# Performance work log

Hardware: AMD Instinct MI355X
Metric: run time of the kernel (lower is better)

Reference implementation:

```python
import jax, jax.numpy as jnp
import numpy as np

B, T, N, L = 128, 2048, 64, 256
NEG = -1e30  # safe -inf surrogate (avoids inf-inf NaNs in gradients)


def setup_inputs() -> dict:
    key = jax.random.key(0)
    k1, k2, k3, k4 = jax.random.split(key, 4)
    inputs = jax.random.normal(k1, (B, T, N), dtype=jnp.float32)
    target = jax.random.randint(k2, (B, L), 0, N, dtype=jnp.int32)
    # valid target lengths in [1, L]
    target_size = jax.random.randint(k3, (B,), 1, L + 1, dtype=jnp.int32)
    # module initializes trans to zeros; use small random values for a nontrivial reference
    trans = jax.random.normal(k4, (N, N), dtype=jnp.float32) * 0.1
    return {"input": inputs, "target": target, "target_size": target_size, "trans": trans}


def _fcc(inputs, trans):
    # Full-connection (partition) score: logsumexp over ALL label paths.
    # alpha_t[b, j] = input[b, t, j] + logsumexp_i( alpha_{t-1}[b, i] + trans[j, i] )
    def step(alpha, x_t):  # alpha: [B, N], x_t: [B, N]
        alpha = x_t + jax.nn.logsumexp(alpha[:, None, :] + trans[None, :, :], axis=2)
        return alpha, None

    alpha0 = inputs[:, 0, :]
    xs = jnp.swapaxes(inputs, 0, 1)[1:]  # [T-1, B, N]
    alphaT, _ = jax.lax.scan(step, alpha0, xs)
    return jax.nn.logsumexp(alphaT, axis=1)  # [B]


def _fac(inputs, trans, target, target_size):
    # Forced-alignment score: logsumexp over alignments emitting target labels
    # in order, each repeated >= 1 time (ASG: no blank).
    b = inputs.shape[0]
    b_idx = jnp.arange(b)
    trans_self = trans[target, target]                 # [B, L] stay on label l
    trans_move = trans[target[:, 1:], target[:, :-1]]  # [B, L-1] advance l-1 -> l
    neg_col = jnp.full((b, 1), NEG, dtype=inputs.dtype)

    alpha0 = jnp.full(target.shape, NEG, dtype=inputs.dtype)
    alpha0 = alpha0.at[:, 0].set(inputs[b_idx, 0, target[:, 0]])

    def step(alpha, x_t):  # alpha: [B, L], x_t: [B, N]
        emit = jnp.take_along_axis(x_t, target, axis=1)  # [B, L]
        stay = alpha + trans_self
        move = jnp.concatenate([neg_col, alpha[:, :-1] + trans_move], axis=1)
        alpha = emit + jnp.logaddexp(stay, move)
        return alpha, None

    xs = jnp.swapaxes(inputs, 0, 1)[1:]  # [T-1, B, N]
    alphaT, _ = jax.lax.scan(step, alpha0, xs)
    return alphaT[b_idx, target_size - 1]  # [B]


def reference(input, target, target_size, trans):
    # ASG loss = FullConnection (partition) - ForceAlignment (target score), per batch element.
    return _fcc(input, trans) - _fac(input, trans, target, target_size)
```

## Files before the change

### kernel.cpp

```cpp
#include <hip/hip_runtime.h>

#define B_ 128
#define T_ 2048
#define N_ 64
#define L_ 256
#define NEGV (-1e30f)
#define PITCH 72
#define LOG2E 1.4426950408889634f
#define LN2   0.6931471805599453f

typedef short  s16x4 __attribute__((ext_vector_type(4)));
typedef short  s16x8 __attribute__((ext_vector_type(8)));
typedef float  f32x4 __attribute__((ext_vector_type(4)));
typedef float  f32x16 __attribute__((ext_vector_type(16)));
typedef unsigned int u32x2 __attribute__((ext_vector_type(2)));
typedef unsigned int u32x4 __attribute__((ext_vector_type(4)));

__device__ __forceinline__ short f2bf_rne(float f) {
    unsigned u = __float_as_uint(f);
    unsigned r = (u + 0x7FFFu + ((u >> 16) & 1u)) >> 16;
    return (short)r;
}
__device__ __forceinline__ float bf2f(unsigned short u) {
    return __uint_as_float(((unsigned)u) << 16);
}
__device__ __forceinline__ float bperm(int byteaddr, float v) {
    return __int_as_float(__builtin_amdgcn_ds_bpermute(byteaddr, __float_as_int(v)));
}
__device__ __forceinline__ float lse2b(float p, float q) {
    float mx = fmaxf(p, q);
    float t  = __builtin_amdgcn_exp2f(-fabsf(p - q));
    return mx + __builtin_amdgcn_logf(1.f + t);
}
__device__ __forceinline__ unsigned cvtpk_bf16(float lo, float hi) {
    unsigned r;
    asm("v_cvt_pk_bf16_f32 %0, %1, %2" : "=v"(r) : "v"(lo), "v"(hi));
    return r;
}
__device__ __forceinline__ void plswap32(unsigned &x, unsigned &y) {
    asm("v_permlane32_swap_b32 %0, %1" : "+v"(x), "+v"(y));
}

__global__ __launch_bounds__(256, 2) void asg_k1(
    const float* __restrict__ x,
    const int*   __restrict__ target,
    const int*   __restrict__ tsize,
    const float* __restrict__ trans,
    float* __restrict__ ws_c,
    unsigned short* __restrict__ ws_R,
    float* __restrict__ ws_v,
    float* __restrict__ ws_w)
{
    __shared__ float evbuf[4][N_];
    const int wid  = threadIdx.x >> 6;
    const int lane = threadIdx.x & 63;
    const int W    = blockIdx.x * 4 + wid;

    if (W < 128) {
        const int b  = W;
        const float* __restrict__ xb = x + (size_t)b * T_ * N_;
        const int l0 = lane * 4;
        int tga[4]; float slf[4], mv[4], a[4];
        #pragma unroll
        for (int j = 0; j < 4; ++j) {
            const int tv = target[b * L_ + l0 + j];
            tga[j] = tv << 2;
            slf[j] = trans[tv * N_ + tv] * LOG2E;
            if (j > 0) mv[j] = trans[tv * N_ + (target[b * L_ + l0 + j - 1])] * LOG2E;
            a[j] = NEGV;
        }
        const int tR  = target[b * L_ + ((l0 - 1 >= 0) ? l0 - 1 : 0)];
        const int tR1 = target[b * L_ + ((l0 - 2 >= 0) ? l0 - 2 : 0)];
        const int tgR = tR << 2;
        const float slfR = trans[tR * N_ + tR] * LOG2E;
        const float mvR  = trans[tR * N_ + tR1] * LOG2E;
        mv[0] = trans[(tga[0] >> 2) * N_ + tR] * LOG2E;
        if (lane == 0) a[0] = xb[tga[0] >> 2] * LOG2E;
        float red = NEGV;
        const int upA = ((lane == 0) ? 0 : lane - 1) << 2;

        float xr[16];
        #pragma unroll
        for (int i = 0; i < 16; ++i) xr[i] = xb[(size_t)(1 + i) * N_ + lane];
        float sc = xr[0] * LOG2E;
        float eR = bperm(tgR, sc);
        float e0 = bperm(tga[0], sc), e1 = bperm(tga[1], sc),
              e2 = bperm(tga[2], sc), e3 = bperm(tga[3], sc);
        float bp = bperm(upA, a[2]);

        #define FWD_STEP(i, rp, RF)                                             \
        {                                                                       \
            const float ceR = eR, c0 = e0, c1 = e1, c2 = e2, c3 = e3;           \
            float scn = xr[((i) + 1) & 15] * LOG2E;                             \
            eR = bperm(tgR, scn);                                               \
            e0 = bperm(tga[0], scn); e1 = bperm(tga[1], scn);                   \
            e2 = bperm(tga[2], scn); e3 = bperm(tga[3], scn);                   \
            if (RF) xr[i] = (rp)[lane];                                         \
            const float n0 = lse2b(a[0] + slf[0], red  + mv[0]) + c0;           \
            const float n1 = lse2b(a[1] + slf[1], a[0] + mv[1]) + c1;           \
            const float n2 = lse2b(a[2] + slf[2], a[1] + mv[2]) + c2;           \
            const float n3 = lse2b(a[3] + slf[3], a[2] + mv[3]) + c3;           \
            const float nr = lse2b(red + slfR,    bp   + mvR)   + ceR;          \
            bp = bperm(upA, n2);                                                \
            a[0] = n0; a[1] = n1; a[2] = n2; a[3] = n3;                         \
            red = (lane == 0) ? NEGV : nr;                                      \
        }
        for (int u = 0; u < 63; ++u) {
            const float* __restrict__ xp = xb + (size_t)(16 * u + 17) * N_;
            #pragma unroll
            for (int i = 0; i < 16; ++i) FWD_STEP(i, xp + i * N_, true);
        }
        #pragma unroll
        for (int i = 0; i < 15; ++i) FWD_STEP(i, xb, false);
        #undef FWD_STEP
        *(float4*)(ws_v + b * 256 + l0) = make_float4(a[0], a[1], a[2], a[3]);
    } else if (W < 256) {
        const int b  = W - 128;
        const float* __restrict__ xb = x + (size_t)b * T_ * N_;
        const int l0 = lane * 4;
        const int lt = tsize[b] - 1;
        int tga[4]; float slf[4], mvin[4], a[4];
        #pragma unroll
        for (int j = 0; j < 4; ++j) {
            const int tv = target[b * L_ + l0 + j];
            tga[j] = tv << 2;
            slf[j] = trans[tv * N_ + tv] * LOG2E;
            if (j > 0) mvin[j] = trans[tv * N_ + (target[b * L_ + l0 + j - 1])] * LOG2E;
            a[j] = (l0 + j == lt) ? 0.f : NEGV;
        }
        const int tR  = target[b * L_ + ((l0 + 4 <= L_ - 1) ? l0 + 4 : L_ - 1)];
        const int tR2 = target[b * L_ + ((l0 + 5 <= L_ - 1) ? l0 + 5 : L_ - 1)];
        const int tgR = tR << 2, tgR2 = tR2 << 2;
        const float slfR = trans[tR * N_ + tR] * LOG2E;
        const float mvR  = trans[tR * N_ + (tga[3] >> 2)] * LOG2E;
        const float mvR2 = trans[tR2 * N_ + tR] * LOG2E;
        float red = (l0 + 4 == lt) ? 0.f : NEGV;
        const int dnA = ((lane == 63) ? 63 : lane + 1) << 2;

        float xr[16];
        #pragma unroll
        for (int i = 0; i < 16; ++i) xr[i] = xb[(size_t)(2047 - i) * N_ + lane];
        float sc = xr[0] * LOG2E;
        float eR = bperm(tgR, sc), eR2 = bperm(tgR2, sc);
        float e0 = bperm(tga[0], sc), e1 = bperm(tga[1], sc),
              e2 = bperm(tga[2], sc), e3 = bperm(tga[3], sc);
        float bp = bperm(dnA, a[1]);

        #define BWD_STEP(i, rp, RF)                                             \
        {                                                                       \
            const float ceR = eR, ceR2 = eR2, c0 = e0, c1 = e1, c2 = e2, c3 = e3;\
            float scn = xr[((i) + 1) & 15] * LOG2E;                             \
            eR = bperm(tgR, scn); eR2 = bperm(tgR2, scn);                       \
            e0 = bperm(tga[0], scn); e1 = bperm(tga[1], scn);                   \
            e2 = bperm(tga[2], scn); e3 = bperm(tga[3], scn);                   \
            if (RF) xr[i] = (rp)[lane];                                         \
            const float t0 = a[0] + c0, t1 = a[1] + c1, t2 = a[2] + c2,         \
                        t3 = a[3] + c3, tr = red + ceR;                         \
            const float n0 = lse2b(t0 + slf[0], t1 + mvin[1]);                  \
            const float n1 = lse2b(t1 + slf[1], t2 + mvin[2]);                  \
            const float n2 = lse2b(t2 + slf[2], t3 + mvin[3]);                  \
            const float n3 = lse2b(t3 + slf[3], tr + mvR);                      \
            const float nr = lse2b(tr + slfR, bp + ceR2 + mvR2);                \
            bp = bperm(dnA, n1);                                                \
            a[0] = n0; a[1] = n1; a[2] = n2; a[3] = n3;                         \
            red = (lane == 63) ? NEGV : nr;                                     \
        }
        for (int u = 0; u < 63; ++u) {
            const float* __restrict__ xp = xb + (size_t)(2047 - 16 * u - 16) * N_;
            #pragma unroll
            for (int i = 0; i < 16; ++i) BWD_STEP(i, xp - (size_t)i * N_, true);
        }
        #pragma unroll
        for (int i = 0; i < 16; ++i) BWD_STEP(i, xb, false);
        #undef BWD_STEP
        *(float4*)(ws_w + b * 256 + l0) = make_float4(a[0], a[1], a[2], a[3]);
    } else {
        const int task = W - 256;
        const int b = task >> 5, k = task & 31;
        const int lane31 = lane & 31, hi = lane >> 5;
        const float* __restrict__ xb = x + (size_t)b * T_ * N_;
        const int t0 = k * 64;
        float* __restrict__ evb = evbuf[wid];

        s16x8 Ahat[2][4];
        float rsum[2];
        #pragma unroll
        for (int r = 0; r < 2; ++r) {
            float rs = 0.f;
            const float* tp = trans + (32 * r + lane31) * N_;
            #pragma unroll
            for (int kt = 0; kt < 4; ++kt) {
                const float* tq = tp + 16 * kt + 8 * hi;
                float4 ta = *(const float4*)tq;
                float4 tb = *(const float4*)(tq + 4);
                float v0 = __expf(ta.x), v1 = __expf(ta.y),
                      v2 = __expf(ta.z), v3 = __expf(ta.w);
                float v4 = __expf(tb.x), v5 = __expf(tb.y),
                      v6 = __expf(tb.z), v7 = __expf(tb.w);
                s16x8 af;
                af[0] = f2bf_rne(v0); af[1] = f2bf_rne(v1);
                af[2] = f2bf_rne(v2); af[3] = f2bf_rne(v3);
                af[4] = f2bf_rne(v4); af[5] = f2bf_rne(v5);
                af[6] = f2bf_rne(v6); af[7] = f2bf_rne(v7);
                rs += ((v0 + v1) + (v2 + v3)) + ((v4 + v5) + (v6 + v7));
                Ahat[r][kt] = af;
            }
            rsum[r] = rs;
        }
        rsum[0] += __shfl_xor(rsum[0], 32);
        rsum[1] += __shfl_xor(rsum[1], 32);
        float rmax = fmaxf(rsum[0], rsum[1]);
        #pragma unroll
        for (int o = 16; o > 0; o >>= 1) rmax = fmaxf(rmax, __shfl_xor(rmax, o));
        const float LS = __logf(rmax);

        s16x8 Pf[4][2];
        #pragma unroll
        for (int kt = 0; kt < 4; ++kt)
            #pragma unroll
            for (int c = 0; c < 2; ++c) {
                s16x8 pf;
                #pragma unroll
                for (int j = 0; j < 8; ++j)
                    pf[j] = (16 * kt + 8 * hi + j == 32 * c + lane31)
                              ? (short)0x3F80 : (short)0;
                Pf[kt][c] = pf;
            }

        const f32x16 z16 = {};
        f32x16 Y00 = {}, Y01 = {}, Y10 = {}, Y11 = {};
        float xpre[4];
        #pragma unroll
        for (int d = 0; d < 4; ++d)
            xpre[d] = xb[(size_t)(t0 + 1 + d) * N_ + lane];
        float c_acc = 0.f;

        #define MM(af, bf, cf) __builtin_amdgcn_mfma_f32_32x32x16_bf16(af, bf, cf, 0, 0, 0)
        #define REDIST(kt, c, Yv)                                               \
        {                                                                       \
            unsigned P0 = cvtpk_bf16(Yv[8*((kt)&1) + 0], Yv[8*((kt)&1) + 1]);   \
            unsigned P1 = cvtpk_bf16(Yv[8*((kt)&1) + 2], Yv[8*((kt)&1) + 3]);   \
            unsigned Q0 = cvtpk_bf16(Yv[8*((kt)&1) + 4], Yv[8*((kt)&1) + 5]);   \
            unsigned Q1 = cvtpk_bf16(Yv[8*((kt)&1) + 6], Yv[8*((kt)&1) + 7]);   \
            plswap32(P0, Q0); plswap32(P1, Q1);                                 \
            u32x4 uv; uv[0] = P0; uv[1] = P1; uv[2] = Q0; uv[3] = Q1;           \
            Pf[kt][c] = __builtin_bit_cast(s16x8, uv);                          \
        }

        #pragma unroll 1
        for (int u = 0; u < 16; ++u) {
            #pragma unroll
            for (int i = 0; i < 4; ++i) {
                const int s = 4 * u + i;
                const int t = t0 + 1 + s;
                if (t < T_) {
                    const float xt = xpre[i];
                    int tp2 = t + 4; if (tp2 > T_ - 1) tp2 = T_ - 1;
                    xpre[i] = xb[(size_t)tp2 * N_ + lane];
                    const float gt = __uint_as_float(
                        __builtin_amdgcn_readfirstlane(__float_as_uint(xt))) + LS;
                    c_acc += gt;
                    evb[lane] = __expf(xt - gt);
                    float4 E[2][4];
                    #pragma unroll
                    for (int r = 0; r < 2; ++r)
                        #pragma unroll
                        for (int q = 0; q < 4; ++q)
                            E[r][q] = *(const float4*)&evb[32 * r + 8 * q + 4 * hi];
                    Y00 = MM(Ahat[0][0], Pf[0][0], z16);
                    Y01 = MM(Ahat[0][0], Pf[0][1], z16);
                    Y10 = MM(Ahat[1][0], Pf[0][0], z16);
                    Y11 = MM(Ahat[1][0], Pf[0][1], z16);
                    #pragma unroll
                    for (int kt = 1; kt < 4; ++kt) {
                        Y00 = MM(Ahat[0][kt], Pf[kt][0], Y00);
                        Y01 = MM(Ahat[0][kt], Pf[kt][1], Y01);
                        Y10 = MM(Ahat[1][kt], Pf[kt][0], Y10);
                        Y11 = MM(Ahat[1][kt], Pf[kt][1], Y11);
                    }
                    #pragma unroll
                    for (int q = 0; q < 4; ++q) {
                        Y00[4*q+0] *= E[0][q].x; Y00[4*q+1] *= E[0][q].y;
                        Y00[4*q+2] *= E[0][q].z; Y00[4*q+3] *= E[0][q].w;
                        Y01[4*q+0] *= E[0][q].x; Y01[4*q+1] *= E[0][q].y;
                        Y01[4*q+2] *= E[0][q].z; Y01[4*q+3] *= E[0][q].w;
                        Y10[4*q+0] *= E[1][q].x; Y10[4*q+1] *= E[1][q].y;
                        Y10[4*q+2] *= E[1][q].z; Y10[4*q+3] *= E[1][q].w;
                        Y11[4*q+0] *= E[1][q].x; Y11[4*q+1] *= E[1][q].y;
                        Y11[4*q+2] *= E[1][q].z; Y11[4*q+3] *= E[1][q].w;
                    }
                    REDIST(0, 0, Y00); REDIST(0, 1, Y01);
                    REDIST(1, 0, Y00); REDIST(1, 1, Y01);
                    REDIST(2, 0, Y10); REDIST(2, 1, Y11);
                    REDIST(3, 0, Y10); REDIST(3, 1, Y11);
                }
            }
        }
        #undef REDIST
        #undef MM

        unsigned short* dst = ws_R + (size_t)(b * 32 + k) * 4096;
        #pragma unroll
        for (int q = 0; q < 4; ++q)
            #pragma unroll
            for (int m = 0; m < 4; ++m) {
                const int reg = 4 * q + m;
                const int rw  = 8 * q + 4 * hi + m;
                dst[(rw     ) * 64 + lane31     ] = (unsigned short)f2bf_rne(Y00[reg]);
                dst[(rw     ) * 64 + 32 + lane31] = (unsigned short)f2bf_rne(Y01[reg]);
                dst[(32 + rw) * 64 + lane31     ] = (unsigned short)f2bf_rne(Y10[reg]);
                dst[(32 + rw) * 64 + 32 + lane31] = (unsigned short)f2bf_rne(Y11[reg]);
            }
        if (lane == 0) ws_c[b * 32 + k] = c_acc;
    }
}

__global__ __launch_bounds__(128) void asg_k2(
    const float* __restrict__ x,
    const float* __restrict__ ws_c,
    const unsigned short* __restrict__ ws_R,
    const float* __restrict__ ws_v,
    const float* __restrict__ ws_w,
    float* __restrict__ out)
{
    __shared__ short rb[2][N_ * PITCH];
    __shared__ __align__(16) float sa[N_];
    __shared__ float sres[2];
    const int b = blockIdx.x, tid = threadIdx.x, lane = tid & 63;

    if (tid < 64) {
        float a0 = x[(size_t)b * T_ * N_ + lane];
        float m0 = a0;
        #pragma unroll
        for (int o = 32; o > 0; o >>= 1) m0 = fmaxf(m0, __shfl_xor(m0, o));
        float  a  = __expf(a0 - m0);
        double Cd = (double)m0;

        const unsigned short* Rb = ws_R + (size_t)b * 32 * 4096;
        const int frow = (lane >> 3), fcol = (lane & 7) * 8;
        {
            #pragma unroll
            for (int q = 0; q < 8; ++q) {
                s16x8 v = *(const s16x8*)(Rb + lane * 8 + 512 * q);
                *(s16x8*)&rb[0][(frow + 8 * q) * PITCH + fcol] = v;
            }
        }
        for (int kk = 0; kk < 32; ++kk) {
            const int kn = (kk < 31) ? kk + 1 : 31;
            s16x8 nv[8];
            #pragma unroll
            for (int q = 0; q < 8; ++q)
                nv[q] = *(const s16x8*)(Rb + (size_t)kn * 4096 + lane * 8 + 512 * q);

            sa[lane] = a;
            float4 sav[16];
            #pragma unroll
            for (int q = 0; q < 16; ++q) sav[q] = ((const float4*)sa)[q];

            float acc4[4] = {0.f, 0.f, 0.f, 0.f};
            #pragma unroll
            for (int u = 0; u < 8; ++u) {
                s16x8 rr = *(const s16x8*)&rb[kk & 1][lane * PITCH + u * 8];
                const float4 s0 = sav[2 * u], s1 = sav[2 * u + 1];
                acc4[0] = fmaf(bf2f((unsigned short)rr[0]), s0.x, acc4[0]);
                acc4[1] = fmaf(bf2f((unsigned short)rr[1]), s0.y, acc4[1]);
                acc4[2] = fmaf(bf2f((unsigned short)rr[2]), s0.z, acc4[2]);
                acc4[3] = fmaf(bf2f((unsigned short)rr[3]), s0.w, acc4[3]);
                acc4[0] = fmaf(bf2f((unsigned short)rr[4]), s1.x, acc4[0]);
                acc4[1] = fmaf(bf2f((unsigned short)rr[5]), s1.y, acc4[1]);
                acc4[2] = fmaf(bf2f((unsigned short)rr[6]), s1.z, acc4[2]);
                acc4[3] = fmaf(bf2f((unsigned short)rr[7]), s1.w, acc4[3]);
            }
            float acc = (acc4[0] + acc4[1]) + (acc4[2] + acc4[3]);
            float rm = acc;
            #pragma unroll
            for (int o = 32; o > 0; o >>= 1) rm = fmaxf(rm, __shfl_xor(rm, o));
            a = acc / rm;
            Cd += (double)(__logf(rm) + ws_c[b * 32 + kk]);

            #pragma unroll
            for (int q = 0; q < 8; ++q)
                *(s16x8*)&rb[(kk + 1) & 1][(frow + 8 * q) * PITCH + fcol] = nv[q];
        }
        float ssum = a;
        #pragma unroll
        for (int o = 32; o > 0; o >>= 1) ssum += __shfl_xor(ssum, o);
        if (lane == 0) sres[0] = (float)(Cd + (double)__logf(ssum));
    } else {
        float4 v4 = ((const float4*)(ws_v + b * 256))[lane];
        float4 w4 = ((const float4*)(ws_w + b * 256))[lane];
        const float s0 = v4.x + w4.x, s1 = v4.y + w4.y,
                    s2 = v4.z + w4.z, s3 = v4.w + w4.w;
        float m = fmaxf(fmaxf(s0, s1), fmaxf(s2, s3));
        #pragma unroll
        for (int o = 32; o > 0; o >>= 1) m = fmaxf(m, __shfl_xor(m, o));
        float sum = __builtin_amdgcn_exp2f(s0 - m) + __builtin_amdgcn_exp2f(s1 - m)
                  + __builtin_amdgcn_exp2f(s2 - m) + __builtin_amdgcn_exp2f(s3 - m);
        #pragma unroll
        for (int o = 32; o > 0; o >>= 1) sum += __shfl_xor(sum, o);
        if (lane == 0) sres[1] = (m + __builtin_amdgcn_logf(sum)) * LN2;
    }
    __syncthreads();
    if (tid == 0) out[b] = sres[0] - sres[1];
}

extern "C" void kernel_launch(void* const* d_in, const int* in_sizes, int n_in,
                              void* d_out, int out_size, void* d_ws, size_t ws_size,
                              hipStream_t stream) {
    (void)in_sizes; (void)n_in; (void)out_size; (void)ws_size;
    const float* xin    = (const float*)d_in[0];
    const int*   target = (const int*)  d_in[1];
    const int*   tsz    = (const int*)  d_in[2];
    const float* trans  = (const float*)d_in[3];
    float* out = (float*)d_out;

    float*          ws_c = (float*)d_ws;
    unsigned short* ws_R = (unsigned short*)((char*)d_ws + 16384);
    float*          ws_v = (float*)((char*)d_ws + 16384 + 33554432);
    float*          ws_w = (float*)((char*)d_ws + 16384 + 33554432 + 131072);

    asg_k1<<<dim3(1088), dim3(256), 0, stream>>>(xin, target, tsz, trans,
                                                 ws_c, ws_R, ws_v, ws_w);
    asg_k2<<<dim3(B_), dim3(128), 0, stream>>>(xin, ws_c, ws_R, ws_v, ws_w, out);
}
```

Before: 286.3 us.

## Spread FAC waves one per block, gather emissions directly, deepen K2 prefetch

The forced-alignment forward and backward waves now get one block each (wave 0 of blocks 0-255), and the FCC chunk tasks are remapped onto the remaining waves. Inside the alignment recurrence, the per-lane coalesced row load plus five or six ds_bpermute shuffles per step is replaced by direct gathered global loads of the needed emission values, prefetched four steps ahead in a register ring. The LOG2E scaling is folded into an fma. In the K2 combine loop, bf16 R tiles are now prefetched two iterations ahead with two register buffers, to hide global-load latency. The gather loads are uncoalesced and raise register use, and isolating the latency-bound waves changes occupancy and block balance.

```diff
diff --git a/kernel.cpp b/kernel.cpp
--- a/kernel.cpp
+++ b/kernel.cpp
@@ -54,128 +54,130 @@
     __shared__ float evbuf[4][N_];
     const int wid  = threadIdx.x >> 6;
     const int lane = threadIdx.x & 63;
-    const int W    = blockIdx.x * 4 + wid;
-
-    if (W < 128) {
-        const int b  = W;
+    const int bx   = blockIdx.x;
+    const bool isfac = (bx < 256) && (wid == 0);
+
+    if (isfac && bx < 128) {
+        const int b  = bx;
         const float* __restrict__ xb = x + (size_t)b * T_ * N_;
         const int l0 = lane * 4;
-        int tga[4]; float slf[4], mv[4], a[4];
+        int tg[4]; float slf[4], mv[4], a[4];
         #pragma unroll
         for (int j = 0; j < 4; ++j) {
             const int tv = target[b * L_ + l0 + j];
-            tga[j] = tv << 2;
+            tg[j] = tv;
             slf[j] = trans[tv * N_ + tv] * LOG2E;
             if (j > 0) mv[j] = trans[tv * N_ + (target[b * L_ + l0 + j - 1])] * LOG2E;
             a[j] = NEGV;
         }
         const int tR  = target[b * L_ + ((l0 - 1 >= 0) ? l0 - 1 : 0)];
         const int tR1 = target[b * L_ + ((l0 - 2 >= 0) ? l0 - 2 : 0)];
-        const int tgR = tR << 2;
         const float slfR = trans[tR * N_ + tR] * LOG2E;
         const float mvR  = trans[tR * N_ + tR1] * LOG2E;
-        mv[0] = trans[(tga[0] >> 2) * N_ + tR] * LOG2E;
-        if (lane == 0) a[0] = xb[tga[0] >> 2] * LOG2E;
+        mv[0] = trans[tg[0] * N_ + tR] * LOG2E;
+        if (lane == 0) a[0] = xb[tg[0]] * LOG2E;
         float red = NEGV;
+        float bp  = NEGV;
         const int upA = ((lane == 0) ? 0 : lane - 1) << 2;
 
-        float xr[16];
-        #pragma unroll
-        for (int i = 0; i < 16; ++i) xr[i] = xb[(size_t)(1 + i) * N_ + lane];
-        float sc = xr[0] * LOG2E;
-        float eR = bperm(tgR, sc);
-        float e0 = bperm(tga[0], sc), e1 = bperm(tga[1], sc),
-              e2 = bperm(tga[2], sc), e3 = bperm(tga[3], sc);
-        float bp = bperm(upA, a[2]);
-
-        #define FWD_STEP(i, rp, RF)                                             \
+        float E[4][5];
+        #pragma unroll
+        for (int d = 0; d < 4; ++d) {
+            const float* __restrict__ xp = xb + (size_t)(1 + d) * N_;
+            E[d][0] = xp[tg[0]]; E[d][1] = xp[tg[1]];
+            E[d][2] = xp[tg[2]]; E[d][3] = xp[tg[3]];
+            E[d][4] = xp[tR];
+        }
+
+        #define FWD_STEP(t, i)                                                  \
         {                                                                       \
-            const float ceR = eR, c0 = e0, c1 = e1, c2 = e2, c3 = e3;           \
-            float scn = xr[((i) + 1) & 15] * LOG2E;                             \
-            eR = bperm(tgR, scn);                                               \
-            e0 = bperm(tga[0], scn); e1 = bperm(tga[1], scn);                   \
-            e2 = bperm(tga[2], scn); e3 = bperm(tga[3], scn);                   \
-            if (RF) xr[i] = (rp)[lane];                                         \
-            const float n0 = lse2b(a[0] + slf[0], red  + mv[0]) + c0;           \
-            const float n1 = lse2b(a[1] + slf[1], a[0] + mv[1]) + c1;           \
-            const float n2 = lse2b(a[2] + slf[2], a[1] + mv[2]) + c2;           \
-            const float n3 = lse2b(a[3] + slf[3], a[2] + mv[3]) + c3;           \
-            const float nr = lse2b(red + slfR,    bp   + mvR)   + ceR;          \
+            const float c0 = E[i][0], c1 = E[i][1], c2 = E[i][2],               \
+                        c3 = E[i][3], cR = E[i][4];                             \
+            const int rw = ((t) + 4 <= 1023) ? (t) + 4 : 1023;                  \
+            const float* __restrict__ xp = xb + (size_t)rw * N_;                \
+            E[i][0] = xp[tg[0]]; E[i][1] = xp[tg[1]];                           \
+            E[i][2] = xp[tg[2]]; E[i][3] = xp[tg[3]];                           \
+            E[i][4] = xp[tR];                                                   \
+            const float n0 = fmaf(c0, LOG2E, lse2b(a[0] + slf[0], red  + mv[0]));\
+            const float n1 = fmaf(c1, LOG2E, lse2b(a[1] + slf[1], a[0] + mv[1]));\
+            const float n2 = fmaf(c2, LOG2E, lse2b(a[2] + slf[2], a[1] + mv[2]));\
+            const float n3 = fmaf(c3, LOG2E, lse2b(a[3] + slf[3], a[2] + mv[3]));\
+            const float nr = fmaf(cR, LOG2E, lse2b(red + slfR,    bp   + mvR)); \
             bp = bperm(upA, n2);                                                \
             a[0] = n0; a[1] = n1; a[2] = n2; a[3] = n3;                         \
             red = (lane == 0) ? NEGV : nr;                                      \
         }
-        for (int u = 0; u < 63; ++u) {
-            const float* __restrict__ xp = xb + (size_t)(16 * u + 17) * N_;
-            #pragma unroll
-            for (int i = 0; i < 16; ++i) FWD_STEP(i, xp + i * N_, true);
-        }
-        #pragma unroll
-        for (int i = 0; i < 15; ++i) FWD_STEP(i, xb, false);
+        for (int u = 0; u < 255; ++u) {
+            const int tb = 1 + 4 * u;
+            #pragma unroll
+            for (int i = 0; i < 4; ++i) FWD_STEP(tb + i, i);
+        }
+        FWD_STEP(1021, 0); FWD_STEP(1022, 1); FWD_STEP(1023, 2);
         #undef FWD_STEP
         *(float4*)(ws_v + b * 256 + l0) = make_float4(a[0], a[1], a[2], a[3]);
-    } else if (W < 256) {
-        const int b  = W - 128;
+    } else if (isfac) {
+        const int b  = bx - 128;
         const float* __restrict__ xb = x + (size_t)b * T_ * N_;
         const int l0 = lane * 4;
         const int lt = tsize[b] - 1;
-        int tga[4]; float slf[4], mvin[4], a[4];
+        int tg[4]; float slf[4], mvin[4], a[4];
         #pragma unroll
         for (int j = 0; j < 4; ++j) {
             const int tv = target[b * L_ + l0 + j];
-            tga[j] = tv << 2;
+            tg[j] = tv;
             slf[j] = trans[tv * N_ + tv] * LOG2E;
             if (j > 0) mvin[j] = trans[tv * N_ + (target[b * L_ + l0 + j - 1])] * LOG2E;
             a[j] = (l0 + j == lt) ? 0.f : NEGV;
         }
         const int tR  = target[b * L_ + ((l0 + 4 <= L_ - 1) ? l0 + 4 : L_ - 1)];
         const int tR2 = target[b * L_ + ((l0 + 5 <= L_ - 1) ? l0 + 5 : L_ - 1)];
-        const int tgR = tR << 2, tgR2 = tR2 << 2;
         const float slfR = trans[tR * N_ + tR] * LOG2E;
-        const float mvR  = trans[tR * N_ + (tga[3] >> 2)] * LOG2E;
+        const float mvR  = trans[tR * N_ + tg[3]] * LOG2E;
         const float mvR2 = trans[tR2 * N_ + tR] * LOG2E;
         float red = (l0 + 4 == lt) ? 0.f : NEGV;
+        float bp  = (l0 + 5 == lt) ? 0.f : NEGV;
         const int dnA = ((lane == 63) ? 63 : lane + 1) << 2;
 
-        float xr[16];
-        #pragma unroll
-        for (int i = 0; i < 16; ++i) xr[i] = xb[(size_t)(2047 - i) * N_ + lane];
-        float sc = xr[0] * LOG2E;
-        float eR = bperm(tgR, sc), eR2 = bperm(tgR2, sc);
-        float e0 = bperm(tga[0], sc), e1 = bperm(tga[1], sc),
-              e2 = bperm(tga[2], sc), e3 = bperm(tga[3], sc);
-        float bp = bperm(dnA, a[1]);
-
-        #define BWD_STEP(i, rp, RF)                                             \
+        float E[4][6];
+        #pragma unroll
+        for (int d = 0; d < 4; ++d) {
+            const float* __restrict__ xp = xb + (size_t)(2047 - d) * N_;
+            E[d][0] = xp[tg[0]]; E[d][1] = xp[tg[1]];
+            E[d][2] = xp[tg[2]]; E[d][3] = xp[tg[3]];
+            E[d][4] = xp[tR];    E[d][5] = xp[tR2];
+        }
+
+        #define BWD_STEP(t, i)                                                  \
         {                                                                       \
-            const float ceR = eR, ceR2 = eR2, c0 = e0, c1 = e1, c2 = e2, c3 = e3;\
-            float scn = xr[((i) + 1) & 15] * LOG2E;                             \
-            eR = bperm(tgR, scn); eR2 = bperm(tgR2, scn);                       \
-            e0 = bperm(tga[0], scn); e1 = bperm(tga[1], scn);                   \
-            e2 = bperm(tga[2], scn); e3 = bperm(tga[3], scn);                   \
-            if (RF) xr[i] = (rp)[lane];                                         \
-            const float t0 = a[0] + c0, t1 = a[1] + c1, t2 = a[2] + c2,         \
-                        t3 = a[3] + c3, tr = red + ceR;                         \
+            const float c0 = E[i][0], c1 = E[i][1], c2 = E[i][2],               \
+                        c3 = E[i][3], cR = E[i][4], cR2 = E[i][5];              \
+            const int rw = ((t) - 4 >= 1024) ? (t) - 4 : 1024;                  \
+            const float* __restrict__ xp = xb + (size_t)rw * N_;                \
+            E[i][0] = xp[tg[0]]; E[i][1] = xp[tg[1]];                           \
+            E[i][2] = xp[tg[2]]; E[i][3] = xp[tg[3]];                           \
+            E[i][4] = xp[tR];    E[i][5] = xp[tR2];                             \
+            const float t0 = fmaf(c0, LOG2E, a[0]), t1 = fmaf(c1, LOG2E, a[1]); \
+            const float t2 = fmaf(c2, LOG2E, a[2]), t3 = fmaf(c3, LOG2E, a[3]); \
+            const float tr = fmaf(cR, LOG2E, red);                              \
             const float n0 = lse2b(t0 + slf[0], t1 + mvin[1]);                  \
             const float n1 = lse2b(t1 + slf[1], t2 + mvin[2]);                  \
             const float n2 = lse2b(t2 + slf[2], t3 + mvin[3]);                  \
             const float n3 = lse2b(t3 + slf[3], tr + mvR);                      \
-            const float nr = lse2b(tr + slfR, bp + ceR2 + mvR2);                \
+            const float nr = lse2b(tr + slfR, bp + fmaf(cR2, LOG2E, mvR2));     \
             bp = bperm(dnA, n1);                                                \
             a[0] = n0; a[1] = n1; a[2] = n2; a[3] = n3;                         \
             red = (lane == 63) ? NEGV : nr;                                     \
         }
-        for (int u = 0; u < 63; ++u) {
-            const float* __restrict__ xp = xb + (size_t)(2047 - 16 * u - 16) * N_;
-            #pragma unroll
-            for (int i = 0; i < 16; ++i) BWD_STEP(i, xp - (size_t)i * N_, true);
-        }
-        #pragma unroll
-        for (int i = 0; i < 16; ++i) BWD_STEP(i, xb, false);
+        for (int u = 0; u < 256; ++u) {
+            const int tb = 2047 - 4 * u;
+            #pragma unroll
+            for (int i = 0; i < 4; ++i) BWD_STEP(tb - i, i);
+        }
         #undef BWD_STEP
         *(float4*)(ws_w + b * 256 + l0) = make_float4(a[0], a[1], a[2], a[3]);
     } else {
-        const int task = W - 256;
+        const int task = (bx < 256) ? (bx * 3 + wid - 1)
+                                    : (768 + (bx - 256) * 4 + wid);
         const int b = task >> 5, k = task & 31;
         const int lane31 = lane & 31, hi = lane >> 5;
         const float* __restrict__ xb = x + (size_t)b * T_ * N_;
@@ -345,22 +347,20 @@
                 *(s16x8*)&rb[0][(frow + 8 * q) * PITCH + fcol] = v;
             }
         }
-        for (int kk = 0; kk < 32; ++kk) {
-            const int kn = (kk < 31) ? kk + 1 : 31;
-            s16x8 nv[8];
-            #pragma unroll
-            for (int q = 0; q < 8; ++q)
-                nv[q] = *(const s16x8*)(Rb + (size_t)kn * 4096 + lane * 8 + 512 * q);
-
+        s16x8 nvA[8], nvB[8];
+        #pragma unroll
+        for (int q = 0; q < 8; ++q)
+            nvA[q] = *(const s16x8*)(Rb + (size_t)4096 + lane * 8 + 512 * q);
+
+        auto k2_step = [&](int kk, int bufi) {
             sa[lane] = a;
             float4 sav[16];
             #pragma unroll
             for (int q = 0; q < 16; ++q) sav[q] = ((const float4*)sa)[q];
-
             float acc4[4] = {0.f, 0.f, 0.f, 0.f};
             #pragma unroll
             for (int u = 0; u < 8; ++u) {
-                s16x8 rr = *(const s16x8*)&rb[kk & 1][lane * PITCH + u * 8];
+                s16x8 rr = *(const s16x8*)&rb[bufi][lane * PITCH + u * 8];
                 const float4 s0 = sav[2 * u], s1 = sav[2 * u + 1];
                 acc4[0] = fmaf(bf2f((unsigned short)rr[0]), s0.x, acc4[0]);
                 acc4[1] = fmaf(bf2f((unsigned short)rr[1]), s0.y, acc4[1]);
@@ -377,10 +377,25 @@
             for (int o = 32; o > 0; o >>= 1) rm = fmaxf(rm, __shfl_xor(rm, o));
             a = acc / rm;
             Cd += (double)(__logf(rm) + ws_c[b * 32 + kk]);
-
+        };
+
+        for (int kk = 0; kk < 32; kk += 2) {
+            const int kA = (kk + 2 < 32) ? kk + 2 : 31;
             #pragma unroll
             for (int q = 0; q < 8; ++q)
-                *(s16x8*)&rb[(kk + 1) & 1][(frow + 8 * q) * PITCH + fcol] = nv[q];
+                nvB[q] = *(const s16x8*)(Rb + (size_t)kA * 4096 + lane * 8 + 512 * q);
+            k2_step(kk, kk & 1);
+            #pragma unroll
+            for (int q = 0; q < 8; ++q)
+                *(s16x8*)&rb[(kk + 1) & 1][(frow + 8 * q) * PITCH + fcol] = nvA[q];
+            const int kB = (kk + 3 < 32) ? kk + 3 : 31;
+            #pragma unroll
+            for (int q = 0; q < 8; ++q)
+                nvA[q] = *(const s16x8*)(Rb + (size_t)kB * 4096 + lane * 8 + 512 * q);
+            k2_step(kk + 1, (kk + 1) & 1);
+            #pragma unroll
+            for (int q = 0; q < 8; ++q)
+                *(s16x8*)&rb[kk & 1][(frow + 8 * q) * PITCH + fcol] = nvB[q];
         }
         float ssum = a;
         #pragma unroll
```

New measurement: 337.0 us. 1.18x slower.

## Give each FAC recurrence its own block and prefetch two R tiles ahead

Applied to the files above, without the earlier changes.

Changes the work-to-wave mapping in k1 so that each of the 256 forward/backward FAC waves runs as wave 0 of its own block. The remaining three waves of those blocks, plus the later blocks, take the FCC chunk tasks. The aim is to spread the long serial FAC recurrences across more CUs instead of packing four into one block, where they compete for a SIMD/CU. In the second kernel, the global-load prefetch of R tiles is restructured to double-register buffering two steps ahead, to hide global latency. The cost is more register pressure and a more complex task index mapping, which must still cover every task exactly.

```diff
diff --git a/kernel.cpp b/kernel.cpp
--- a/kernel.cpp
+++ b/kernel.cpp
@@ -54,10 +54,11 @@
     __shared__ float evbuf[4][N_];
     const int wid  = threadIdx.x >> 6;
     const int lane = threadIdx.x & 63;
-    const int W    = blockIdx.x * 4 + wid;
-
-    if (W < 128) {
-        const int b  = W;
+    const int bx   = blockIdx.x;
+    const bool isfac = (bx < 256) && (wid == 0);
+
+    if (isfac && bx < 128) {
+        const int b  = bx;
         const float* __restrict__ xb = x + (size_t)b * T_ * N_;
         const int l0 = lane * 4;
         int tga[4]; float slf[4], mv[4], a[4];
@@ -114,8 +115,8 @@
         for (int i = 0; i < 15; ++i) FWD_STEP(i, xb, false);
         #undef FWD_STEP
         *(float4*)(ws_v + b * 256 + l0) = make_float4(a[0], a[1], a[2], a[3]);
-    } else if (W < 256) {
-        const int b  = W - 128;
+    } else if (isfac) {
+        const int b  = bx - 128;
         const float* __restrict__ xb = x + (size_t)b * T_ * N_;
         const int l0 = lane * 4;
         const int lt = tsize[b] - 1;
@@ -175,7 +176,8 @@
         #undef BWD_STEP
         *(float4*)(ws_w + b * 256 + l0) = make_float4(a[0], a[1], a[2], a[3]);
     } else {
-        const int task = W - 256;
+        const int task = (bx < 256) ? (bx * 3 + wid - 1)
+                                    : (768 + (bx - 256) * 4 + wid);
         const int b = task >> 5, k = task & 31;
         const int lane31 = lane & 31, hi = lane >> 5;
         const float* __restrict__ xb = x + (size_t)b * T_ * N_;
@@ -345,22 +347,20 @@
                 *(s16x8*)&rb[0][(frow + 8 * q) * PITCH + fcol] = v;
             }
         }
-        for (int kk = 0; kk < 32; ++kk) {
-            const int kn = (kk < 31) ? kk + 1 : 31;
-            s16x8 nv[8];
-            #pragma unroll
-            for (int q = 0; q < 8; ++q)
-                nv[q] = *(const s16x8*)(Rb + (size_t)kn * 4096 + lane * 8 + 512 * q);
-
+        s16x8 nvA[8], nvB[8];
+        #pragma unroll
+        for (int q = 0; q < 8; ++q)
+            nvA[q] = *(const s16x8*)(Rb + (size_t)4096 + lane * 8 + 512 * q);
+
+        auto k2_step = [&](int kk, int bufi) {
             sa[lane] = a;
             float4 sav[16];
             #pragma unroll
             for (int q = 0; q < 16; ++q) sav[q] = ((const float4*)sa)[q];
-
             float acc4[4] = {0.f, 0.f, 0.f, 0.f};
             #pragma unroll
             for (int u = 0; u < 8; ++u) {
-                s16x8 rr = *(const s16x8*)&rb[kk & 1][lane * PITCH + u * 8];
+                s16x8 rr = *(const s16x8*)&rb[bufi][lane * PITCH + u * 8];
                 const float4 s0 = sav[2 * u], s1 = sav[2 * u + 1];
                 acc4[0] = fmaf(bf2f((unsigned short)rr[0]), s0.x, acc4[0]);
                 acc4[1] = fmaf(bf2f((unsigned short)rr[1]), s0.y, acc4[1]);
@@ -377,10 +377,25 @@
             for (int o = 32; o > 0; o >>= 1) rm = fmaxf(rm, __shfl_xor(rm, o));
             a = acc / rm;
             Cd += (double)(__logf(rm) + ws_c[b * 32 + kk]);
-
+        };
+
+        for (int kk = 0; kk < 32; kk += 2) {
+            const int kA = (kk + 2 < 32) ? kk + 2 : 31;
             #pragma unroll
             for (int q = 0; q < 8; ++q)
-                *(s16x8*)&rb[(kk + 1) & 1][(frow + 8 * q) * PITCH + fcol] = nv[q];
+                nvB[q] = *(const s16x8*)(Rb + (size_t)kA * 4096 + lane * 8 + 512 * q);
+            k2_step(kk, kk & 1);
+            #pragma unroll
+            for (int q = 0; q < 8; ++q)
+                *(s16x8*)&rb[(kk + 1) & 1][(frow + 8 * q) * PITCH + fcol] = nvA[q];
+            const int kB = (kk + 3 < 32) ? kk + 3 : 31;
+            #pragma unroll
+            for (int q = 0; q < 8; ++q)
+                nvA[q] = *(const s16x8*)(Rb + (size_t)kB * 4096 + lane * 8 + 512 * q);
+            k2_step(kk + 1, (kk + 1) & 1);
+            #pragma unroll
+            for (int q = 0; q < 8; ++q)
+                *(s16x8*)&rb[kk & 1][(frow + 8 * q) * PITCH + fcol] = nvB[q];
         }
         float ssum = a;
         #pragma unroll
```

Result: slower. 316.9 us (+10.7%).
